# Kernel optimization log

Hardware: AMD Instinct MI355X
Metric: run time of the kernel (lower is better)

Reference implementation:

```python
import jax, jax.numpy as jnp
import numpy as np

NUM_EXPERTS = 8
HIDDEN = 1024
INTER = 1024
BATCH = 2
SEQ = 1024
TOP_K = 2
SWIGLU_ALPHA = 1.702
LIMIT = 7.0


def setup_inputs() -> dict:
    key = jax.random.key(0)
    ks = jax.random.split(key, 7)
    hidden_states = jax.random.normal(ks[0], (BATCH, SEQ, HIDDEN), jnp.float32)
    router_indices = jax.random.randint(ks[1], (BATCH * SEQ, TOP_K), 0, NUM_EXPERTS)
    routing_weights = jax.nn.softmax(
        jax.random.normal(ks[2], (BATCH * SEQ, NUM_EXPERTS), jnp.float32), axis=-1)
    scale = 0.02
    gate_up_proj = jax.random.normal(ks[3], (NUM_EXPERTS, HIDDEN, 2 * INTER), jnp.float32) * scale
    gate_up_proj_bias = jax.random.normal(ks[4], (NUM_EXPERTS, 2 * INTER), jnp.float32) * scale
    down_proj = jax.random.normal(ks[5], (NUM_EXPERTS, INTER, HIDDEN), jnp.float32) * scale
    down_proj_bias = jax.random.normal(ks[6], (NUM_EXPERTS, HIDDEN), jnp.float32) * scale
    return {
        "hidden_states": hidden_states,
        "router_indices": router_indices,
        "routing_weights": routing_weights,
        "gate_up_proj": gate_up_proj,
        "gate_up_proj_bias": gate_up_proj_bias,
        "down_proj": down_proj,
        "down_proj_bias": down_proj_bias,
    }


def _grouped_mm(x, w, expert_ids):
    """Grouped GEMM: y[t] = x[t] @ w[expert_ids[t]].

    x: [T, K], w: [E, K, N], expert_ids: [T] int.
    Reference form via one-hot masking (exact equivalent of torch._grouped_mm
    on expert-sorted tokens); guaranteed jit- and grad-safe.
    """
    onehot = jax.nn.one_hot(expert_ids, w.shape[0], dtype=x.dtype)  # [T, E]
    y_all = jnp.einsum('tk,ekn->etn', x, w)                         # [E, T, N]
    return jnp.einsum('te,etn->tn', onehot, y_all)                  # [T, N]


def _gpt_oss_swiglu(x):
    gate = jnp.minimum(x[..., ::2], LIMIT)
    up = jnp.clip(x[..., 1::2], -LIMIT, LIMIT)
    glu = gate * jax.nn.sigmoid(gate * SWIGLU_ALPHA)
    return (up + 1.0) * glu


def reference(hidden_states, router_indices, routing_weights,
              gate_up_proj, gate_up_proj_bias, down_proj, down_proj_bias):
    B = hidden_states.shape[0]
    H = hidden_states.shape[-1]
    x = hidden_states.reshape(-1, H)                       # [M, H]
    M = x.shape[0]
    top_k = router_indices.shape[1]
    num_experts = gate_up_proj.shape[0]

    # routing_weights is [M, num_experts] -> gather the top-k weights
    topk_weights = jnp.take_along_axis(routing_weights, router_indices, axis=1)  # [M, K]

    flat_experts = router_indices.reshape(-1)              # [T = M*K]
    sort_idx = jnp.argsort(flat_experts)                   # expert-sorted order
    sorted_pos = sort_idx // top_k                         # token id per slot
    expert_sorted = flat_experts[sort_idx]                 # [T]
    grouped = x[sorted_pos]                                # [T, H]

    gate_up = _grouped_mm(grouped, gate_up_proj, expert_sorted)
    gate_up = gate_up + gate_up_proj_bias[expert_sorted]   # per-expert bias
    inter = _gpt_oss_swiglu(gate_up)                       # [T, I]

    down = _grouped_mm(inter, down_proj, expert_sorted)
    down = down + down_proj_bias[expert_sorted]            # [T, H]
    down = down * topk_weights.reshape(-1)[sort_idx][:, None]

    out = jnp.zeros((M, H), x.dtype).at[sorted_pos].add(down)  # scatter-add combine
    return out.reshape(B, -1, H)
```

## Files before the change

### kernel.cpp

```cpp
#include <hip/hip_runtime.h>

#define NE 8
#define NH 1024
#define NI 1024
#define NGU 2048
#define MTOK 2048
#define TSLOT 4096

#define MAXT64 80
#define MAXT128 40

typedef short s16x8 __attribute__((ext_vector_type(8)));
typedef float f32x4 __attribute__((ext_vector_type(4)));
typedef unsigned short u16;

#define WS_SEG      0
#define WS_DESC64   64
#define WS_DESC128  384
#define WS_SLOT     1024
#define WS_POS      17408
#define WS_INTER    33792
#define WS_AREG     8422400UL
#define WS_WREG     25199616UL
#define WS_NEED_FAST 58754048UL

__device__ inline u16 f2bf(float f) {
    unsigned u = __builtin_bit_cast(unsigned, f);
    u += 0x7fffu + ((u >> 16) & 1u);
    return (u16)(u >> 16);
}

__device__ inline void lds_dma16(const u16* g, u16* l) {
    __builtin_amdgcn_global_load_lds(
        (const __attribute__((address_space(1))) unsigned int*)g,
        (__attribute__((address_space(3))) unsigned int*)l, 16, 0, 0);
}

__device__ inline int lds_off(int row, int blk) {
    return (row << 7) | (((blk ^ (row & 7)) & 7) << 4);
}

#define PIPE_FENCE asm volatile("" ::: "memory")
#define WAIT_VM6   asm volatile("s_waitcnt vmcnt(6)" ::: "memory")
#define WAIT_VM0   asm volatile("s_waitcnt vmcnt(0)" ::: "memory")

__global__ void k_build(const int* __restrict__ ridx, int* __restrict__ seg,
                        int* __restrict__ d64, int* __restrict__ d128,
                        int* __restrict__ slot_of, int* __restrict__ pos_of) {
    __shared__ int cnt[NE];
    __shared__ int cur[NE];
    int tid = threadIdx.x;
    if (tid < NE) cnt[tid] = 0;
    __syncthreads();
    for (int s = tid; s < TSLOT; s += blockDim.x) atomicAdd(&cnt[ridx[s] & 7], 1);
    __syncthreads();
    if (tid == 0) {
        int a = 0;
        for (int e = 0; e < NE; ++e) { seg[e] = a; cur[e] = a; a += cnt[e]; }
        seg[NE] = a;
        int nt = 0;
        for (int e = 0; e < NE; ++e)
            for (int m0 = 0; m0 < cnt[e]; m0 += 64) d64[nt++] = (e << 16) | (m0 / 64);
        for (; nt < MAXT64; ++nt) d64[nt] = -1;
        nt = 0;
        for (int e = 0; e < NE; ++e)
            for (int m0 = 0; m0 < cnt[e]; m0 += 128) d128[nt++] = (e << 16) | (m0 / 128);
        for (; nt < MAXT128; ++nt) d128[nt] = -1;
    }
    __syncthreads();
    for (int s = tid; s < TSLOT; s += blockDim.x) {
        int e = ridx[s] & 7;
        int p = atomicAdd(&cur[e], 1);
        slot_of[p] = s;
        pos_of[s] = p;
    }
}

__global__ __launch_bounds__(256) void k_gather(const float* __restrict__ x,
                                                const int* __restrict__ slot_of,
                                                u16* __restrict__ A) {
    int r = blockIdx.x;
    int token = slot_of[r] >> 1;
    float4 v = ((const float4*)(x + (size_t)token * NH))[threadIdx.x];
    ushort4 o;
    o.x = f2bf(v.x); o.y = f2bf(v.y); o.z = f2bf(v.z); o.w = f2bf(v.w);
    ((ushort4*)(A + (size_t)r * NH))[threadIdx.x] = o;
}

__global__ __launch_bounds__(256) void k_tr(const float* __restrict__ W,
                                            u16* __restrict__ WT, int K, int N) {
    __shared__ u16 T[64][66];
    int tid = threadIdx.x;
    const float* in = W + (size_t)blockIdx.z * K * N;
    u16* out = WT + (size_t)blockIdx.z * N * K;
    int n0 = blockIdx.x * 64, k0 = blockIdx.y * 64;
#pragma unroll
    for (int p = 0; p < 2; ++p) {
        int kr = p * 32 + (tid >> 4) * 2;
        int nc = (tid & 15) * 4;
        const float* r0 = in + (size_t)(k0 + kr) * N + n0 + nc;
        float4 v0 = *(const float4*)r0;
        float4 v1 = *(const float4*)(r0 + N);
#pragma unroll
        for (int i = 0; i < 4; ++i) {
            unsigned lo = f2bf(((const float*)&v0)[i]);
            unsigned hi = f2bf(((const float*)&v1)[i]);
            *(unsigned*)&T[nc + i][kr] = lo | (hi << 16);
        }
    }
    __syncthreads();
#pragma unroll
    for (int p = 0; p < 2; ++p) {
        int idx = p * 256 + tid;
        int nr = idx >> 3, kc = (idx & 7) * 8;
        unsigned q0 = *(const unsigned*)&T[nr][kc + 0];
        unsigned q1 = *(const unsigned*)&T[nr][kc + 2];
        unsigned q2 = *(const unsigned*)&T[nr][kc + 4];
        unsigned q3 = *(const unsigned*)&T[nr][kc + 6];
        uint4 vv = {q0, q1, q2, q3};
        *(uint4*)(out + (size_t)(n0 + nr) * K + k0 + kc) = vv;
    }
}

__global__ __launch_bounds__(256) void k_gateup_f(
        const u16* __restrict__ A,
        const u16* __restrict__ wt,
        const float* __restrict__ bias,
        const int* __restrict__ seg, const int* __restrict__ desc,
        u16* __restrict__ inter) {
    int d = desc[blockIdx.x];
    if (d < 0) return;
    int e = d >> 16, mt = d & 0xffff;
    int seg0 = seg[e], Te = seg[e + 1] - seg0, m0 = mt * 128;

    __shared__ __align__(16) u16 As0[128 * 64];
    __shared__ __align__(16) u16 As1[128 * 64];
    __shared__ __align__(16) u16 Bs0[64 * 64];
    __shared__ __align__(16) u16 Bs1[64 * 64];

    int tid = threadIdx.x;
    int lane = tid & 63, w = tid >> 6;
    int ml = lane & 15, kq = lane >> 4;
    int wm = w >> 1, wn = w & 1;
    int n0 = blockIdx.y * 64;
    const u16* wte = wt + (size_t)e * NGU * NH;
    int dr = lane >> 3, db = (lane & 7) ^ dr;

    const u16* aptr[4];
#pragma unroll
    for (int c = 0; c < 4; ++c) {
        int gr = seg0 + m0 + c * 32 + w * 8 + dr;
        if (gr > TSLOT - 1) gr = TSLOT - 1;
        aptr[c] = A + (size_t)gr * NH + db * 8;
    }
    const u16* bptr[2];
#pragma unroll
    for (int c = 0; c < 2; ++c)
        bptr[c] = wte + (size_t)(n0 + c * 32 + w * 8 + dr) * NH + db * 8;

    auto stage = [&](u16* AS, u16* BS, int kb) {
#pragma unroll
        for (int c = 0; c < 4; ++c) lds_dma16(aptr[c] + kb, AS + c * 2048 + w * 512);
#pragma unroll
        for (int c = 0; c < 2; ++c) lds_dma16(bptr[c] + kb, BS + c * 2048 + w * 512);
    };

    f32x4 zero = {0.f, 0.f, 0.f, 0.f};
    f32x4 acc[4][2];
#pragma unroll
    for (int i = 0; i < 4; ++i) { acc[i][0] = zero; acc[i][1] = zero; }

    auto compute = [&](const u16* AS, const u16* BS) {
#pragma unroll
        for (int kk = 0; kk < 64; kk += 32) {
            s16x8 af[4], bf[2];
#pragma unroll
            for (int i = 0; i < 4; ++i)
                af[i] = *(const s16x8*)((const char*)AS + lds_off(wm * 64 + i * 16 + ml, (kk >> 3) + kq));
#pragma unroll
            for (int i = 0; i < 2; ++i)
                bf[i] = *(const s16x8*)((const char*)BS + lds_off(wn * 32 + i * 16 + ml, (kk >> 3) + kq));
#pragma unroll
            for (int mi = 0; mi < 4; ++mi)
#pragma unroll
                for (int ni = 0; ni < 2; ++ni)
                    acc[mi][ni] = __builtin_amdgcn_mfma_f32_16x16x32_bf16(
                        af[mi], bf[ni], acc[mi][ni], 0, 0, 0);
        }
    };

    stage(As0, Bs0, 0);
    for (int t = 0; t < 16; t += 2) {
        stage(As1, Bs1, (t + 1) << 6);
        WAIT_VM6;
        __builtin_amdgcn_s_barrier();
        PIPE_FENCE;
        __builtin_amdgcn_s_setprio(1);
        compute(As0, Bs0);
        __builtin_amdgcn_s_setprio(0);
        PIPE_FENCE;
        __builtin_amdgcn_s_barrier();
        if (t < 14) {
            stage(As0, Bs0, (t + 2) << 6);
            WAIT_VM6;
        } else {
            WAIT_VM0;
        }
        __builtin_amdgcn_s_barrier();
        PIPE_FENCE;
        __builtin_amdgcn_s_setprio(1);
        compute(As1, Bs1);
        __builtin_amdgcn_s_setprio(0);
        PIPE_FENCE;
        __builtin_amdgcn_s_barrier();
    }

#pragma unroll
    for (int ni = 0; ni < 2; ++ni) {
        int n = n0 + wn * 32 + ni * 16 + ml;
        float bv = bias[e * NGU + n];
#pragma unroll
        for (int mi = 0; mi < 4; ++mi) {
#pragma unroll
            for (int r = 0; r < 4; ++r) {
                float v = acc[mi][ni][r] + bv;
                float pr = __shfl_xor(v, 1, 64);
                float g = (lane & 1) ? pr : v;
                float u = (lane & 1) ? v : pr;
                g = fminf(g, 7.0f);
                u = fminf(fmaxf(u, -7.0f), 7.0f);
                float glu = g / (1.0f + __expf(-1.702f * g));
                float y = (u + 1.0f) * glu;
                int mloc = wm * 64 + mi * 16 + kq * 4 + r;
                if (!(lane & 1) && (m0 + mloc) < Te)
                    inter[(size_t)(seg0 + m0 + mloc) * NI + (n >> 1)] = f2bf(y);
            }
        }
    }
}

__global__ __launch_bounds__(256) void k_down_f(
        const u16* __restrict__ inter,
        const u16* __restrict__ wt,
        const float* __restrict__ bias,
        const float* __restrict__ rw,
        const int* __restrict__ seg, const int* __restrict__ desc,
        const int* __restrict__ slot_of,
        float* __restrict__ out) {
    int d = desc[blockIdx.x];
    if (d < 0) return;
    int e = d >> 16, mt = d & 0xffff;
    int seg0 = seg[e], Te = seg[e + 1] - seg0, m0 = mt * 128;
    int kz = blockIdx.z;

    __shared__ __align__(16) u16 As0[128 * 64];
    __shared__ __align__(16) u16 As1[128 * 64];
    __shared__ __align__(16) u16 Bs0[64 * 64];
    __shared__ __align__(16) u16 Bs1[64 * 64];
    __shared__ int tokS[128];
    __shared__ float wgtS[128];

    int tid = threadIdx.x;
    if (tid < 128) {
        int m = m0 + tid;
        if (m < Te) {
            int token = slot_of[seg0 + m] >> 1;
            tokS[tid] = token;
            wgtS[tid] = rw[token * NE + e];
        } else {
            tokS[tid] = 0;
            wgtS[tid] = 0.0f;
        }
    }

    int lane = tid & 63, w = tid >> 6;
    int ml = lane & 15, kq = lane >> 4;
    int wm = w >> 1, wn = w & 1;
    int n0 = blockIdx.y * 64;
    const u16* wte = wt + (size_t)e * NH * NI;
    int dr = lane >> 3, db = (lane & 7) ^ dr;
    int kbeg = kz * (NI / 2);

    const u16* aptr[4];
#pragma unroll
    for (int c = 0; c < 4; ++c) {
        int gr = seg0 + m0 + c * 32 + w * 8 + dr;
        if (gr > TSLOT - 1) gr = TSLOT - 1;
        aptr[c] = inter + (size_t)gr * NI + db * 8;
    }
    const u16* bptr[2];
#pragma unroll
    for (int c = 0; c < 2; ++c)
        bptr[c] = wte + (size_t)(n0 + c * 32 + w * 8 + dr) * NI + db * 8;

    auto stage = [&](u16* AS, u16* BS, int kb) {
#pragma unroll
        for (int c = 0; c < 4; ++c) lds_dma16(aptr[c] + kb, AS + c * 2048 + w * 512);
#pragma unroll
        for (int c = 0; c < 2; ++c) lds_dma16(bptr[c] + kb, BS + c * 2048 + w * 512);
    };

    f32x4 zero = {0.f, 0.f, 0.f, 0.f};
    f32x4 acc[4][2];
#pragma unroll
    for (int i = 0; i < 4; ++i) { acc[i][0] = zero; acc[i][1] = zero; }

    auto compute = [&](const u16* AS, const u16* BS) {
#pragma unroll
        for (int kk = 0; kk < 64; kk += 32) {
            s16x8 af[4], bf[2];
#pragma unroll
            for (int i = 0; i < 4; ++i)
                af[i] = *(const s16x8*)((const char*)AS + lds_off(wm * 64 + i * 16 + ml, (kk >> 3) + kq));
#pragma unroll
            for (int i = 0; i < 2; ++i)
                bf[i] = *(const s16x8*)((const char*)BS + lds_off(wn * 32 + i * 16 + ml, (kk >> 3) + kq));
#pragma unroll
            for (int mi = 0; mi < 4; ++mi)
#pragma unroll
                for (int ni = 0; ni < 2; ++ni)
                    acc[mi][ni] = __builtin_amdgcn_mfma_f32_16x16x32_bf16(
                        af[mi], bf[ni], acc[mi][ni], 0, 0, 0);
        }
    };

    stage(As0, Bs0, kbeg);
    for (int t = 0; t < 8; t += 2) {
        stage(As1, Bs1, kbeg + ((t + 1) << 6));
        WAIT_VM6;
        __builtin_amdgcn_s_barrier();
        PIPE_FENCE;
        __builtin_amdgcn_s_setprio(1);
        compute(As0, Bs0);
        __builtin_amdgcn_s_setprio(0);
        PIPE_FENCE;
        __builtin_amdgcn_s_barrier();
        if (t < 6) {
            stage(As0, Bs0, kbeg + ((t + 2) << 6));
            WAIT_VM6;
        } else {
            WAIT_VM0;
        }
        __builtin_amdgcn_s_barrier();
        PIPE_FENCE;
        __builtin_amdgcn_s_setprio(1);
        compute(As1, Bs1);
        __builtin_amdgcn_s_setprio(0);
        PIPE_FENCE;
        __builtin_amdgcn_s_barrier();
    }

    float bv[2];
#pragma unroll
    for (int ni = 0; ni < 2; ++ni)
        bv[ni] = kz ? 0.0f : bias[e * NH + n0 + wn * 32 + ni * 16 + ml];

#pragma unroll
    for (int mi = 0; mi < 4; ++mi) {
#pragma unroll
        for (int r = 0; r < 4; ++r) {
            int mloc = wm * 64 + mi * 16 + kq * 4 + r;
            if ((m0 + mloc) < Te) {
                int token = tokS[mloc];
                float wgt = wgtS[mloc];
#pragma unroll
                for (int ni = 0; ni < 2; ++ni) {
                    int n = n0 + wn * 32 + ni * 16 + ml;
                    atomicAdd(&out[(size_t)token * NH + n], (acc[mi][ni][r] + bv[ni]) * wgt);
                }
            }
        }
    }
}

__global__ __launch_bounds__(256) void k_gateup_s(
        const float* __restrict__ x, const float* __restrict__ w,
        const float* __restrict__ bias,
        const int* __restrict__ seg, const int* __restrict__ desc,
        const int* __restrict__ slot_of, u16* __restrict__ inter) {
    int d = desc[blockIdx.x];
    if (d < 0) return;
    int e = d >> 16, mt = d & 0xffff;
    int seg0 = seg[e], Te = seg[e + 1] - seg0, m0 = mt * 64;
    __shared__ u16 As[64 * 40];
    __shared__ int tok[64];
    int tid = threadIdx.x;
    if (tid < 64) {
        int m = m0 + tid;
        tok[tid] = (m < Te) ? (slot_of[seg0 + m] >> 1) : -1;
    }
    __syncthreads();
    int lane = tid & 63, wave = tid >> 6;
    int arow = tid >> 2, acol = (tid & 3) * 8;
    int ta = tok[arow];
    int kq = lane >> 4, ml = lane & 15;
    int nb = blockIdx.y * 128 + wave * 32;
    const float* wp = w + (size_t)e * NH * NGU;
    f32x4 zero = {0.f, 0.f, 0.f, 0.f};
    f32x4 acc[4][2];
#pragma unroll
    for (int i = 0; i < 4; ++i) { acc[i][0] = zero; acc[i][1] = zero; }
    for (int kb = 0; kb < NH; kb += 32) {
        float4 a0 = {0, 0, 0, 0}, a1 = {0, 0, 0, 0};
        if (ta >= 0) {
            const float* xp = x + (size_t)ta * NH + kb + acol;
            a0 = *(const float4*)xp; a1 = *(const float4*)(xp + 4);
        }
        s16x8 av;
        av[0] = (short)f2bf(a0.x); av[1] = (short)f2bf(a0.y);
        av[2] = (short)f2bf(a0.z); av[3] = (short)f2bf(a0.w);
        av[4] = (short)f2bf(a1.x); av[5] = (short)f2bf(a1.y);
        av[6] = (short)f2bf(a1.z); av[7] = (short)f2bf(a1.w);
        __syncthreads();
        *(s16x8*)&As[arow * 40 + acol] = av;
        __syncthreads();
        s16x8 afr[4];
#pragma unroll
        for (int msi = 0; msi < 4; ++msi)
            afr[msi] = *(const s16x8*)&As[(msi * 16 + ml) * 40 + kq * 8];
        s16x8 bfr[2];
#pragma unroll
        for (int s = 0; s < 2; ++s) {
            const float* bp = wp + (size_t)(kb + kq * 8) * NGU + nb + s * 16 + ml;
#pragma unroll
            for (int j = 0; j < 8; ++j) bfr[s][j] = (short)f2bf(bp[(size_t)j * NGU]);
        }
#pragma unroll
        for (int msi = 0; msi < 4; ++msi)
#pragma unroll
            for (int s = 0; s < 2; ++s)
                acc[msi][s] = __builtin_amdgcn_mfma_f32_16x16x32_bf16(
                    afr[msi], bfr[s], acc[msi][s], 0, 0, 0);
    }
#pragma unroll
    for (int s = 0; s < 2; ++s) {
        int n = nb + s * 16 + ml;
        float bv = bias[e * NGU + n];
#pragma unroll
        for (int msi = 0; msi < 4; ++msi) {
#pragma unroll
            for (int r = 0; r < 4; ++r) {
                float v = acc[msi][s][r] + bv;
                float pr = __shfl_xor(v, 1, 64);
                float g = (lane & 1) ? pr : v;
                float u = (lane & 1) ? v : pr;
                g = fminf(g, 7.0f);
                u = fminf(fmaxf(u, -7.0f), 7.0f);
                float glu = g / (1.0f + __expf(-1.702f * g));
                float y = (u + 1.0f) * glu;
                int mrow = m0 + msi * 16 + kq * 4 + r;
                if (!(lane & 1) && mrow < Te)
                    inter[(size_t)(seg0 + mrow) * NI + (n >> 1)] = f2bf(y);
            }
        }
    }
}

__global__ __launch_bounds__(256) void k_down_s(
        const u16* __restrict__ inter, const float* __restrict__ w,
        const float* __restrict__ bias, const float* __restrict__ rw,
        const int* __restrict__ seg, const int* __restrict__ desc,
        const int* __restrict__ slot_of, float* __restrict__ out) {
    int d = desc[blockIdx.x];
    if (d < 0) return;
    int e = d >> 16, mt = d & 0xffff;
    int seg0 = seg[e], Te = seg[e + 1] - seg0, m0 = mt * 64;
    __shared__ u16 As[64 * 40];
    int tid = threadIdx.x;
    int lane = tid & 63, wave = tid >> 6;
    int arow = tid >> 2, acol = (tid & 3) * 8;
    bool avalid = (m0 + arow) < Te;
    int kq = lane >> 4, ml = lane & 15;
    int nb = blockIdx.y * 128 + wave * 32;
    const float* wp = w + (size_t)e * NI * NH;
    f32x4 zero = {0.f, 0.f, 0.f, 0.f};
    f32x4 acc[4][2];
#pragma unroll
    for (int i = 0; i < 4; ++i) { acc[i][0] = zero; acc[i][1] = zero; }
    for (int kb = 0; kb < NI; kb += 32) {
        s16x8 av = {0, 0, 0, 0, 0, 0, 0, 0};
        if (avalid) av = *(const s16x8*)(inter + (size_t)(seg0 + m0 + arow) * NI + kb + acol);
        __syncthreads();
        *(s16x8*)&As[arow * 40 + acol] = av;
        __syncthreads();
        s16x8 afr[4];
#pragma unroll
        for (int msi = 0; msi < 4; ++msi)
            afr[msi] = *(const s16x8*)&As[(msi * 16 + ml) * 40 + kq * 8];
        s16x8 bfr[2];
#pragma unroll
        for (int s = 0; s < 2; ++s) {
            const float* bp = wp + (size_t)(kb + kq * 8) * NH + nb + s * 16 + ml;
#pragma unroll
            for (int j = 0; j < 8; ++j) bfr[s][j] = (short)f2bf(bp[(size_t)j * NH]);
        }
#pragma unroll
        for (int msi = 0; msi < 4; ++msi)
#pragma unroll
            for (int s = 0; s < 2; ++s)
                acc[msi][s] = __builtin_amdgcn_mfma_f32_16x16x32_bf16(
                    afr[msi], bfr[s], acc[msi][s], 0, 0, 0);
    }
    float bv[2];
    bv[0] = bias[e * NH + nb + ml];
    bv[1] = bias[e * NH + nb + 16 + ml];
#pragma unroll
    for (int msi = 0; msi < 4; ++msi) {
#pragma unroll
        for (int r = 0; r < 4; ++r) {
            int mrow = m0 + msi * 16 + kq * 4 + r;
            if (mrow < Te) {
                int slot = slot_of[seg0 + mrow];
                int token = slot >> 1;
                float wgt = rw[token * NE + e];
#pragma unroll
                for (int s = 0; s < 2; ++s) {
                    int n = nb + s * 16 + ml;
                    atomicAdd(&out[(size_t)token * NH + n], (acc[msi][s][r] + bv[s]) * wgt);
                }
            }
        }
    }
}

extern "C" void kernel_launch(void* const* d_in, const int* in_sizes, int n_in,
                              void* d_out, int out_size, void* d_ws, size_t ws_size,
                              hipStream_t stream) {
    const float* x   = (const float*)d_in[0];
    const int*   ri  = (const int*)d_in[1];
    const float* rw  = (const float*)d_in[2];
    const float* wgu = (const float*)d_in[3];
    const float* bgu = (const float*)d_in[4];
    const float* wd  = (const float*)d_in[5];
    const float* bd  = (const float*)d_in[6];
    float* out = (float*)d_out;

    char* ws = (char*)d_ws;
    int* seg     = (int*)(ws + WS_SEG);
    int* d64     = (int*)(ws + WS_DESC64);
    int* d128    = (int*)(ws + WS_DESC128);
    int* slot_of = (int*)(ws + WS_SLOT);
    int* pos_of  = (int*)(ws + WS_POS);
    u16* inter   = (u16*)(ws + WS_INTER);

    hipLaunchKernelGGL(k_build, dim3(1), dim3(256), 0, stream, ri, seg, d64, d128,
                       slot_of, pos_of);
    hipMemsetAsync(out, 0, (size_t)MTOK * NH * sizeof(float), stream);

    if (ws_size >= WS_NEED_FAST) {
        u16* aReg = (u16*)(ws + WS_AREG);
        u16* wReg = (u16*)(ws + WS_WREG);
        hipLaunchKernelGGL(k_tr, dim3(NGU / 64, NH / 64, NE), dim3(256), 0, stream,
                           wgu, wReg, NH, NGU);
        hipLaunchKernelGGL(k_gather, dim3(TSLOT), dim3(256), 0, stream, x, slot_of, aReg);
        hipLaunchKernelGGL(k_gateup_f, dim3(MAXT128, NGU / 64), dim3(256), 0, stream,
                           aReg, wReg, bgu, seg, d128, inter);
        hipLaunchKernelGGL(k_tr, dim3(NH / 64, NI / 64, NE), dim3(256), 0, stream,
                           wd, wReg, NI, NH);
        hipLaunchKernelGGL(k_down_f, dim3(MAXT128, NH / 64, 2), dim3(256), 0, stream,
                           inter, wReg, bd, rw, seg, d128, slot_of, out);
    } else {
        hipLaunchKernelGGL(k_gateup_s, dim3(MAXT64, NGU / 128), dim3(256), 0, stream,
                           x, wgu, bgu, seg, d64, slot_of, inter);
        hipLaunchKernelGGL(k_down_s, dim3(MAXT64, NH / 128), dim3(256), 0, stream,
                           inter, wd, bd, rw, seg, d64, slot_of, out);
    }
}
```

Before: 248.3 us.

## Fuse routing, conversion, zeroing, and weight transposes into fewer launches

Merges routing-table build, bf16 conversion of the activations, output zeroing and the gate_up weight transpose into one prep kernel. The gather now indexes tokens directly through slot_of instead of building a separate expert-sorted copy. The down-projection weight transpose rides as extra blocks in the gate_up GEMM launch when the workspace is large enough. The down GEMM drops its K-split to run one pass over K. This cuts launch count, removes the memset and gather passes, and overlaps weight conversion with compute, at the cost of larger grids and fewer down-GEMM blocks.

After: 222.0 us. 10.6% less time.

```diff
diff --git a/kernel.cpp b/kernel.cpp
--- a/kernel.cpp
+++ b/kernel.cpp
@@ -21,8 +21,10 @@
 #define WS_POS      17408
 #define WS_INTER    33792
 #define WS_AREG     8422400UL
-#define WS_WREG     25199616UL
-#define WS_NEED_FAST 58754048UL
+#define WS_WREG     12616704UL
+#define WS_WTD      46171136UL
+#define WS_NEED_FAST  46171136UL
+#define WS_NEED_PIGGY 62948352UL
 
 __device__ inline u16 f2bf(float f) {
     unsigned u = __builtin_bit_cast(unsigned, f);
@@ -43,6 +45,362 @@
 #define PIPE_FENCE asm volatile("" ::: "memory")
 #define WAIT_VM6   asm volatile("s_waitcnt vmcnt(6)" ::: "memory")
 #define WAIT_VM0   asm volatile("s_waitcnt vmcnt(0)" ::: "memory")
+
+__device__ inline void tr_tile(const float* __restrict__ in, u16* __restrict__ outw,
+                               int K, int N, int n0, int k0, int tid, u16 (*T)[66]) {
+#pragma unroll
+    for (int p = 0; p < 2; ++p) {
+        int kr = p * 32 + (tid >> 4) * 2;
+        int nc = (tid & 15) * 4;
+        const float* r0 = in + (size_t)(k0 + kr) * N + n0 + nc;
+        float4 v0 = *(const float4*)r0;
+        float4 v1 = *(const float4*)(r0 + N);
+#pragma unroll
+        for (int i = 0; i < 4; ++i) {
+            unsigned lo = f2bf(((const float*)&v0)[i]);
+            unsigned hi = f2bf(((const float*)&v1)[i]);
+            *(unsigned*)&T[nc + i][kr] = lo | (hi << 16);
+        }
+    }
+    __syncthreads();
+#pragma unroll
+    for (int p = 0; p < 2; ++p) {
+        int idx = p * 256 + tid;
+        int nr = idx >> 3, kc = (idx & 7) * 8;
+        unsigned q0 = *(const unsigned*)&T[nr][kc + 0];
+        unsigned q1 = *(const unsigned*)&T[nr][kc + 2];
+        unsigned q2 = *(const unsigned*)&T[nr][kc + 4];
+        unsigned q3 = *(const unsigned*)&T[nr][kc + 6];
+        uint4 vv = {q0, q1, q2, q3};
+        *(uint4*)(outw + (size_t)(n0 + nr) * K + k0 + kc) = vv;
+    }
+}
+
+__global__ __launch_bounds__(256) void k_tr(const float* __restrict__ W,
+                                            u16* __restrict__ WT, int K, int N) {
+    __shared__ u16 T[64][66];
+    tr_tile(W + (size_t)blockIdx.z * K * N, WT + (size_t)blockIdx.z * N * K,
+            K, N, blockIdx.x * 64, blockIdx.y * 64, threadIdx.x, T);
+}
+
+__global__ __launch_bounds__(256) void k_prep(
+        const float* __restrict__ x, const int* __restrict__ ridx,
+        const float* __restrict__ wgu,
+        int* __restrict__ seg, int* __restrict__ d64, int* __restrict__ d128,
+        int* __restrict__ slot_of, int* __restrict__ pos_of,
+        u16* __restrict__ A, u16* __restrict__ wt_gu, float* __restrict__ out) {
+    __shared__ int cnt[NE];
+    __shared__ int cur[NE];
+    __shared__ u16 T[64][66];
+    int b = blockIdx.x;
+    int tid = threadIdx.x;
+
+    if (b == 0) {
+        if (tid < NE) cnt[tid] = 0;
+        __syncthreads();
+        for (int s = tid; s < TSLOT; s += blockDim.x) atomicAdd(&cnt[ridx[s] & 7], 1);
+        __syncthreads();
+        if (tid == 0) {
+            int a = 0;
+            for (int e = 0; e < NE; ++e) { seg[e] = a; cur[e] = a; a += cnt[e]; }
+            seg[NE] = a;
+            int nt = 0;
+            for (int e = 0; e < NE; ++e)
+                for (int m0 = 0; m0 < cnt[e]; m0 += 64) d64[nt++] = (e << 16) | (m0 / 64);
+            for (; nt < MAXT64; ++nt) d64[nt] = -1;
+            nt = 0;
+            for (int e = 0; e < NE; ++e)
+                for (int m0 = 0; m0 < cnt[e]; m0 += 128) d128[nt++] = (e << 16) | (m0 / 128);
+            for (; nt < MAXT128; ++nt) d128[nt] = -1;
+        }
+        __syncthreads();
+        for (int s = tid; s < TSLOT; s += blockDim.x) {
+            int e = ridx[s] & 7;
+            int p = atomicAdd(&cur[e], 1);
+            slot_of[p] = s;
+            pos_of[s] = p;
+        }
+    } else if (b <= MTOK) {
+        int t = b - 1;
+        float4 v = ((const float4*)(x + (size_t)t * NH))[tid];
+        ushort4 o;
+        o.x = f2bf(v.x); o.y = f2bf(v.y); o.z = f2bf(v.z); o.w = f2bf(v.w);
+        ((ushort4*)(A + (size_t)t * NH))[tid] = o;
+        float4 z = {0.f, 0.f, 0.f, 0.f};
+        ((float4*)(out + (size_t)t * NH))[tid] = z;
+    } else {
+        int id = b - (MTOK + 1);
+        int e = id >> 9, rem = id & 511;
+        int kblk = rem >> 5, nblk = rem & 31;
+        tr_tile(wgu + (size_t)e * NH * NGU, wt_gu + (size_t)e * NGU * NH,
+                NH, NGU, nblk * 64, kblk * 64, tid, T);
+    }
+}
+
+__global__ __launch_bounds__(256) void k_gateup_f(
+        const u16* __restrict__ A,
+        const u16* __restrict__ wt,
+        const float* __restrict__ bias,
+        const int* __restrict__ seg, const int* __restrict__ desc,
+        const int* __restrict__ slot_of,
+        u16* __restrict__ inter,
+        const float* __restrict__ wd,
+        u16* __restrict__ wtd) {
+    __shared__ __align__(16) char SM[49152];
+    int tid = threadIdx.x;
+
+    if (blockIdx.x >= MAXT128) {
+        int id = (blockIdx.x - MAXT128) * 32 + blockIdx.y;
+        int e = id >> 8, rem = id & 255;
+        int kblk = rem >> 4, nblk = rem & 15;
+        u16 (*T)[66] = (u16(*)[66])SM;
+        tr_tile(wd + (size_t)e * NI * NH, wtd + (size_t)e * NH * NI,
+                NI, NH, nblk * 64, kblk * 64, tid, T);
+        return;
+    }
+
+    int d = desc[blockIdx.x];
+    if (d < 0) return;
+    int e = d >> 16, mt = d & 0xffff;
+    int seg0 = seg[e], Te = seg[e + 1] - seg0, m0 = mt * 128;
+
+    u16* As0 = (u16*)SM;
+    u16* As1 = (u16*)(SM + 16384);
+    u16* Bs0 = (u16*)(SM + 32768);
+    u16* Bs1 = (u16*)(SM + 40960);
+
+    int lane = tid & 63, w = tid >> 6;
+    int ml = lane & 15, kq = lane >> 4;
+    int wm = w >> 1, wn = w & 1;
+    int n0 = blockIdx.y * 64;
+    const u16* wte = wt + (size_t)e * NGU * NH;
+    int dr = lane >> 3, db = (lane & 7) ^ dr;
+
+    const u16* aptr[4];
+#pragma unroll
+    for (int c = 0; c < 4; ++c) {
+        int gr = seg0 + m0 + c * 32 + w * 8 + dr;
+        if (gr > TSLOT - 1) gr = TSLOT - 1;
+        int tok = slot_of[gr] >> 1;
+        aptr[c] = A + (size_t)tok * NH + db * 8;
+    }
+    const u16* bptr[2];
+#pragma unroll
+    for (int c = 0; c < 2; ++c)
+        bptr[c] = wte + (size_t)(n0 + c * 32 + w * 8 + dr) * NH + db * 8;
+
+    auto stage = [&](u16* AS, u16* BS, int kb) {
+#pragma unroll
+        for (int c = 0; c < 4; ++c) lds_dma16(aptr[c] + kb, AS + c * 2048 + w * 512);
+#pragma unroll
+        for (int c = 0; c < 2; ++c) lds_dma16(bptr[c] + kb, BS + c * 2048 + w * 512);
+    };
+
+    f32x4 zero = {0.f, 0.f, 0.f, 0.f};
+    f32x4 acc[4][2];
+#pragma unroll
+    for (int i = 0; i < 4; ++i) { acc[i][0] = zero; acc[i][1] = zero; }
+
+    auto compute = [&](const u16* AS, const u16* BS) {
+#pragma unroll
+        for (int kk = 0; kk < 64; kk += 32) {
+            s16x8 af[4], bf[2];
+#pragma unroll
+            for (int i = 0; i < 4; ++i)
+                af[i] = *(const s16x8*)((const char*)AS + lds_off(wm * 64 + i * 16 + ml, (kk >> 3) + kq));
+#pragma unroll
+            for (int i = 0; i < 2; ++i)
+                bf[i] = *(const s16x8*)((const char*)BS + lds_off(wn * 32 + i * 16 + ml, (kk >> 3) + kq));
+#pragma unroll
+            for (int mi = 0; mi < 4; ++mi)
+#pragma unroll
+                for (int ni = 0; ni < 2; ++ni)
+                    acc[mi][ni] = __builtin_amdgcn_mfma_f32_16x16x32_bf16(
+                        af[mi], bf[ni], acc[mi][ni], 0, 0, 0);
+        }
+    };
+
+    stage(As0, Bs0, 0);
+    for (int t = 0; t < 16; t += 2) {
+        stage(As1, Bs1, (t + 1) << 6);
+        WAIT_VM6;
+        __builtin_amdgcn_s_barrier();
+        PIPE_FENCE;
+        __builtin_amdgcn_s_setprio(1);
+        compute(As0, Bs0);
+        __builtin_amdgcn_s_setprio(0);
+        PIPE_FENCE;
+        __builtin_amdgcn_s_barrier();
+        if (t < 14) {
+            stage(As0, Bs0, (t + 2) << 6);
+            WAIT_VM6;
+        } else {
+            WAIT_VM0;
+        }
+        __builtin_amdgcn_s_barrier();
+        PIPE_FENCE;
+        __builtin_amdgcn_s_setprio(1);
+        compute(As1, Bs1);
+        __builtin_amdgcn_s_setprio(0);
+        PIPE_FENCE;
+        __builtin_amdgcn_s_barrier();
+    }
+
+#pragma unroll
+    for (int ni = 0; ni < 2; ++ni) {
+        int n = n0 + wn * 32 + ni * 16 + ml;
+        float bv = bias[e * NGU + n];
+#pragma unroll
+        for (int mi = 0; mi < 4; ++mi) {
+#pragma unroll
+            for (int r = 0; r < 4; ++r) {
+                float v = acc[mi][ni][r] + bv;
+                float pr = __shfl_xor(v, 1, 64);
+                float g = (lane & 1) ? pr : v;
+                float u = (lane & 1) ? v : pr;
+                g = fminf(g, 7.0f);
+                u = fminf(fmaxf(u, -7.0f), 7.0f);
+                float glu = g / (1.0f + __expf(-1.702f * g));
+                float y = (u + 1.0f) * glu;
+                int mloc = wm * 64 + mi * 16 + kq * 4 + r;
+                if (!(lane & 1) && (m0 + mloc) < Te)
+                    inter[(size_t)(seg0 + m0 + mloc) * NI + (n >> 1)] = f2bf(y);
+            }
+        }
+    }
+}
+
+__global__ __launch_bounds__(256) void k_down_f(
+        const u16* __restrict__ inter,
+        const u16* __restrict__ wt,
+        const float* __restrict__ bias,
+        const float* __restrict__ rw,
+        const int* __restrict__ seg, const int* __restrict__ desc,
+        const int* __restrict__ slot_of,
+        float* __restrict__ out) {
+    int d = desc[blockIdx.x];
+    if (d < 0) return;
+    int e = d >> 16, mt = d & 0xffff;
+    int seg0 = seg[e], Te = seg[e + 1] - seg0, m0 = mt * 128;
+
+    __shared__ __align__(16) u16 As0[128 * 64];
+    __shared__ __align__(16) u16 As1[128 * 64];
+    __shared__ __align__(16) u16 Bs0[64 * 64];
+    __shared__ __align__(16) u16 Bs1[64 * 64];
+    __shared__ int tokS[128];
+    __shared__ float wgtS[128];
+
+    int tid = threadIdx.x;
+    if (tid < 128) {
+        int m = m0 + tid;
+        if (m < Te) {
+            int token = slot_of[seg0 + m] >> 1;
+            tokS[tid] = token;
+            wgtS[tid] = rw[token * NE + e];
+        } else {
+            tokS[tid] = 0;
+            wgtS[tid] = 0.0f;
+        }
+    }
+
+    int lane = tid & 63, w = tid >> 6;
+    int ml = lane & 15, kq = lane >> 4;
+    int wm = w >> 1, wn = w & 1;
+    int n0 = blockIdx.y * 64;
+    const u16* wte = wt + (size_t)e * NH * NI;
+    int dr = lane >> 3, db = (lane & 7) ^ dr;
+
+    const u16* aptr[4];
+#pragma unroll
+    for (int c = 0; c < 4; ++c) {
+        int gr = seg0 + m0 + c * 32 + w * 8 + dr;
+        if (gr > TSLOT - 1) gr = TSLOT - 1;
+        aptr[c] = inter + (size_t)gr * NI + db * 8;
+    }
+    const u16* bptr[2];
+#pragma unroll
+    for (int c = 0; c < 2; ++c)
+        bptr[c] = wte + (size_t)(n0 + c * 32 + w * 8 + dr) * NI + db * 8;
+
+    auto stage = [&](u16* AS, u16* BS, int kb) {
+#pragma unroll
+        for (int c = 0; c < 4; ++c) lds_dma16(aptr[c] + kb, AS + c * 2048 + w * 512);
+#pragma unroll
+        for (int c = 0; c < 2; ++c) lds_dma16(bptr[c] + kb, BS + c * 2048 + w * 512);
+    };
+
+    f32x4 zero = {0.f, 0.f, 0.f, 0.f};
+    f32x4 acc[4][2];
+#pragma unroll
+    for (int i = 0; i < 4; ++i) { acc[i][0] = zero; acc[i][1] = zero; }
+
+    auto compute = [&](const u16* AS, const u16* BS) {
+#pragma unroll
+        for (int kk = 0; kk < 64; kk += 32) {
+            s16x8 af[4], bf[2];
+#pragma unroll
+            for (int i = 0; i < 4; ++i)
+                af[i] = *(const s16x8*)((const char*)AS + lds_off(wm * 64 + i * 16 + ml, (kk >> 3) + kq));
+#pragma unroll
+            for (int i = 0; i < 2; ++i)
+                bf[i] = *(const s16x8*)((const char*)BS + lds_off(wn * 32 + i * 16 + ml, (kk >> 3) + kq));
+#pragma unroll
+            for (int mi = 0; mi < 4; ++mi)
+#pragma unroll
+                for (int ni = 0; ni < 2; ++ni)
+                    acc[mi][ni] = __builtin_amdgcn_mfma_f32_16x16x32_bf16(
+                        af[mi], bf[ni], acc[mi][ni], 0, 0, 0);
+        }
+    };
+
+    stage(As0, Bs0, 0);
+    for (int t = 0; t < 16; t += 2) {
+        stage(As1, Bs1, (t + 1) << 6);
+        WAIT_VM6;
+        __builtin_amdgcn_s_barrier();
+        PIPE_FENCE;
+        __builtin_amdgcn_s_setprio(1);
+        compute(As0, Bs0);
+        __builtin_amdgcn_s_setprio(0);
+        PIPE_FENCE;
+        __builtin_amdgcn_s_barrier();
+        if (t < 14) {
+            stage(As0, Bs0, (t + 2) << 6);
+            WAIT_VM6;
+        } else {
+            WAIT_VM0;
+        }
+        __builtin_amdgcn_s_barrier();
+        PIPE_FENCE;
+        __builtin_amdgcn_s_setprio(1);
+        compute(As1, Bs1);
+        __builtin_amdgcn_s_setprio(0);
+        PIPE_FENCE;
+        __builtin_amdgcn_s_barrier();
+    }
+
+    float bv[2];
+#pragma unroll
+    for (int ni = 0; ni < 2; ++ni)
+        bv[ni] = bias[e * NH + n0 + wn * 32 + ni * 16 + ml];
+
+#pragma unroll
+    for (int mi = 0; mi < 4; ++mi) {
+#pragma unroll
+        for (int r = 0; r < 4; ++r) {
+            int mloc = wm * 64 + mi * 16 + kq * 4 + r;
+            if ((m0 + mloc) < Te) {
+                int token = tokS[mloc];
+                float wgt = wgtS[mloc];
+#pragma unroll
+                for (int ni = 0; ni < 2; ++ni) {
+                    int n = n0 + wn * 32 + ni * 16 + ml;
+                    atomicAdd(&out[(size_t)token * NH + n], (acc[mi][ni][r] + bv[ni]) * wgt);
+                }
+            }
+        }
+    }
+}
 
 __global__ void k_build(const int* __restrict__ ridx, int* __restrict__ seg,
                         int* __restrict__ d64, int* __restrict__ d128,
@@ -76,303 +434,6 @@
     }
 }
 
-__global__ __launch_bounds__(256) void k_gather(const float* __restrict__ x,
-                                                const int* __restrict__ slot_of,
-                                                u16* __restrict__ A) {
-    int r = blockIdx.x;
-    int token = slot_of[r] >> 1;
-    float4 v = ((const float4*)(x + (size_t)token * NH))[threadIdx.x];
-    ushort4 o;
-    o.x = f2bf(v.x); o.y = f2bf(v.y); o.z = f2bf(v.z); o.w = f2bf(v.w);
-    ((ushort4*)(A + (size_t)r * NH))[threadIdx.x] = o;
-}
-
-__global__ __launch_bounds__(256) void k_tr(const float* __restrict__ W,
-                                            u16* __restrict__ WT, int K, int N) {
-    __shared__ u16 T[64][66];
-    int tid = threadIdx.x;
-    const float* in = W + (size_t)blockIdx.z * K * N;
-    u16* out = WT + (size_t)blockIdx.z * N * K;
-    int n0 = blockIdx.x * 64, k0 = blockIdx.y * 64;
-#pragma unroll
-    for (int p = 0; p < 2; ++p) {
-        int kr = p * 32 + (tid >> 4) * 2;
-        int nc = (tid & 15) * 4;
-        const float* r0 = in + (size_t)(k0 + kr) * N + n0 + nc;
-        float4 v0 = *(const float4*)r0;
-        float4 v1 = *(const float4*)(r0 + N);
-#pragma unroll
-        for (int i = 0; i < 4; ++i) {
-            unsigned lo = f2bf(((const float*)&v0)[i]);
-            unsigned hi = f2bf(((const float*)&v1)[i]);
-            *(unsigned*)&T[nc + i][kr] = lo | (hi << 16);
-        }
-    }
-    __syncthreads();
-#pragma unroll
-    for (int p = 0; p < 2; ++p) {
-        int idx = p * 256 + tid;
-        int nr = idx >> 3, kc = (idx & 7) * 8;
-        unsigned q0 = *(const unsigned*)&T[nr][kc + 0];
-        unsigned q1 = *(const unsigned*)&T[nr][kc + 2];
-        unsigned q2 = *(const unsigned*)&T[nr][kc + 4];
-        unsigned q3 = *(const unsigned*)&T[nr][kc + 6];
-        uint4 vv = {q0, q1, q2, q3};
-        *(uint4*)(out + (size_t)(n0 + nr) * K + k0 + kc) = vv;
-    }
-}
-
-__global__ __launch_bounds__(256) void k_gateup_f(
-        const u16* __restrict__ A,
-        const u16* __restrict__ wt,
-        const float* __restrict__ bias,
-        const int* __restrict__ seg, const int* __restrict__ desc,
-        u16* __restrict__ inter) {
-    int d = desc[blockIdx.x];
-    if (d < 0) return;
-    int e = d >> 16, mt = d & 0xffff;
-    int seg0 = seg[e], Te = seg[e + 1] - seg0, m0 = mt * 128;
-
-    __shared__ __align__(16) u16 As0[128 * 64];
-    __shared__ __align__(16) u16 As1[128 * 64];
-    __shared__ __align__(16) u16 Bs0[64 * 64];
-    __shared__ __align__(16) u16 Bs1[64 * 64];
-
-    int tid = threadIdx.x;
-    int lane = tid & 63, w = tid >> 6;
-    int ml = lane & 15, kq = lane >> 4;
-    int wm = w >> 1, wn = w & 1;
-    int n0 = blockIdx.y * 64;
-    const u16* wte = wt + (size_t)e * NGU * NH;
-    int dr = lane >> 3, db = (lane & 7) ^ dr;
-
-    const u16* aptr[4];
-#pragma unroll
-    for (int c = 0; c < 4; ++c) {
-        int gr = seg0 + m0 + c * 32 + w * 8 + dr;
-        if (gr > TSLOT - 1) gr = TSLOT - 1;
-        aptr[c] = A + (size_t)gr * NH + db * 8;
-    }
-    const u16* bptr[2];
-#pragma unroll
-    for (int c = 0; c < 2; ++c)
-        bptr[c] = wte + (size_t)(n0 + c * 32 + w * 8 + dr) * NH + db * 8;
-
-    auto stage = [&](u16* AS, u16* BS, int kb) {
-#pragma unroll
-        for (int c = 0; c < 4; ++c) lds_dma16(aptr[c] + kb, AS + c * 2048 + w * 512);
-#pragma unroll
-        for (int c = 0; c < 2; ++c) lds_dma16(bptr[c] + kb, BS + c * 2048 + w * 512);
-    };
-
-    f32x4 zero = {0.f, 0.f, 0.f, 0.f};
-    f32x4 acc[4][2];
-#pragma unroll
-    for (int i = 0; i < 4; ++i) { acc[i][0] = zero; acc[i][1] = zero; }
-
-    auto compute = [&](const u16* AS, const u16* BS) {
-#pragma unroll
-        for (int kk = 0; kk < 64; kk += 32) {
-            s16x8 af[4], bf[2];
-#pragma unroll
-            for (int i = 0; i < 4; ++i)
-                af[i] = *(const s16x8*)((const char*)AS + lds_off(wm * 64 + i * 16 + ml, (kk >> 3) + kq));
-#pragma unroll
-            for (int i = 0; i < 2; ++i)
-                bf[i] = *(const s16x8*)((const char*)BS + lds_off(wn * 32 + i * 16 + ml, (kk >> 3) + kq));
-#pragma unroll
-            for (int mi = 0; mi < 4; ++mi)
-#pragma unroll
-                for (int ni = 0; ni < 2; ++ni)
-                    acc[mi][ni] = __builtin_amdgcn_mfma_f32_16x16x32_bf16(
-                        af[mi], bf[ni], acc[mi][ni], 0, 0, 0);
-        }
-    };
-
-    stage(As0, Bs0, 0);
-    for (int t = 0; t < 16; t += 2) {
-        stage(As1, Bs1, (t + 1) << 6);
-        WAIT_VM6;
-        __builtin_amdgcn_s_barrier();
-        PIPE_FENCE;
-        __builtin_amdgcn_s_setprio(1);
-        compute(As0, Bs0);
-        __builtin_amdgcn_s_setprio(0);
-        PIPE_FENCE;
-        __builtin_amdgcn_s_barrier();
-        if (t < 14) {
-            stage(As0, Bs0, (t + 2) << 6);
-            WAIT_VM6;
-        } else {
-            WAIT_VM0;
-        }
-        __builtin_amdgcn_s_barrier();
-        PIPE_FENCE;
-        __builtin_amdgcn_s_setprio(1);
-        compute(As1, Bs1);
-        __builtin_amdgcn_s_setprio(0);
-        PIPE_FENCE;
-        __builtin_amdgcn_s_barrier();
-    }
-
-#pragma unroll
-    for (int ni = 0; ni < 2; ++ni) {
-        int n = n0 + wn * 32 + ni * 16 + ml;
-        float bv = bias[e * NGU + n];
-#pragma unroll
-        for (int mi = 0; mi < 4; ++mi) {
-#pragma unroll
-            for (int r = 0; r < 4; ++r) {
-                float v = acc[mi][ni][r] + bv;
-                float pr = __shfl_xor(v, 1, 64);
-                float g = (lane & 1) ? pr : v;
-                float u = (lane & 1) ? v : pr;
-                g = fminf(g, 7.0f);
-                u = fminf(fmaxf(u, -7.0f), 7.0f);
-                float glu = g / (1.0f + __expf(-1.702f * g));
-                float y = (u + 1.0f) * glu;
-                int mloc = wm * 64 + mi * 16 + kq * 4 + r;
-                if (!(lane & 1) && (m0 + mloc) < Te)
-                    inter[(size_t)(seg0 + m0 + mloc) * NI + (n >> 1)] = f2bf(y);
-            }
-        }
-    }
-}
-
-__global__ __launch_bounds__(256) void k_down_f(
-        const u16* __restrict__ inter,
-        const u16* __restrict__ wt,
-        const float* __restrict__ bias,
-        const float* __restrict__ rw,
-        const int* __restrict__ seg, const int* __restrict__ desc,
-        const int* __restrict__ slot_of,
-        float* __restrict__ out) {
-    int d = desc[blockIdx.x];
-    if (d < 0) return;
-    int e = d >> 16, mt = d & 0xffff;
-    int seg0 = seg[e], Te = seg[e + 1] - seg0, m0 = mt * 128;
-    int kz = blockIdx.z;
-
-    __shared__ __align__(16) u16 As0[128 * 64];
-    __shared__ __align__(16) u16 As1[128 * 64];
-    __shared__ __align__(16) u16 Bs0[64 * 64];
-    __shared__ __align__(16) u16 Bs1[64 * 64];
-    __shared__ int tokS[128];
-    __shared__ float wgtS[128];
-
-    int tid = threadIdx.x;
-    if (tid < 128) {
-        int m = m0 + tid;
-        if (m < Te) {
-            int token = slot_of[seg0 + m] >> 1;
-            tokS[tid] = token;
-            wgtS[tid] = rw[token * NE + e];
-        } else {
-            tokS[tid] = 0;
-            wgtS[tid] = 0.0f;
-        }
-    }
-
-    int lane = tid & 63, w = tid >> 6;
-    int ml = lane & 15, kq = lane >> 4;
-    int wm = w >> 1, wn = w & 1;
-    int n0 = blockIdx.y * 64;
-    const u16* wte = wt + (size_t)e * NH * NI;
-    int dr = lane >> 3, db = (lane & 7) ^ dr;
-    int kbeg = kz * (NI / 2);
-
-    const u16* aptr[4];
-#pragma unroll
-    for (int c = 0; c < 4; ++c) {
-        int gr = seg0 + m0 + c * 32 + w * 8 + dr;
-        if (gr > TSLOT - 1) gr = TSLOT - 1;
-        aptr[c] = inter + (size_t)gr * NI + db * 8;
-    }
-    const u16* bptr[2];
-#pragma unroll
-    for (int c = 0; c < 2; ++c)
-        bptr[c] = wte + (size_t)(n0 + c * 32 + w * 8 + dr) * NI + db * 8;
-
-    auto stage = [&](u16* AS, u16* BS, int kb) {
-#pragma unroll
-        for (int c = 0; c < 4; ++c) lds_dma16(aptr[c] + kb, AS + c * 2048 + w * 512);
-#pragma unroll
-        for (int c = 0; c < 2; ++c) lds_dma16(bptr[c] + kb, BS + c * 2048 + w * 512);
-    };
-
-    f32x4 zero = {0.f, 0.f, 0.f, 0.f};
-    f32x4 acc[4][2];
-#pragma unroll
-    for (int i = 0; i < 4; ++i) { acc[i][0] = zero; acc[i][1] = zero; }
-
-    auto compute = [&](const u16* AS, const u16* BS) {
-#pragma unroll
-        for (int kk = 0; kk < 64; kk += 32) {
-            s16x8 af[4], bf[2];
-#pragma unroll
-            for (int i = 0; i < 4; ++i)
-                af[i] = *(const s16x8*)((const char*)AS + lds_off(wm * 64 + i * 16 + ml, (kk >> 3) + kq));
-#pragma unroll
-            for (int i = 0; i < 2; ++i)
-                bf[i] = *(const s16x8*)((const char*)BS + lds_off(wn * 32 + i * 16 + ml, (kk >> 3) + kq));
-#pragma unroll
-            for (int mi = 0; mi < 4; ++mi)
-#pragma unroll
-                for (int ni = 0; ni < 2; ++ni)
-                    acc[mi][ni] = __builtin_amdgcn_mfma_f32_16x16x32_bf16(
-                        af[mi], bf[ni], acc[mi][ni], 0, 0, 0);
-        }
-    };
-
-    stage(As0, Bs0, kbeg);
-    for (int t = 0; t < 8; t += 2) {
-        stage(As1, Bs1, kbeg + ((t + 1) << 6));
-        WAIT_VM6;
-        __builtin_amdgcn_s_barrier();
-        PIPE_FENCE;
-        __builtin_amdgcn_s_setprio(1);
-        compute(As0, Bs0);
-        __builtin_amdgcn_s_setprio(0);
-        PIPE_FENCE;
-        __builtin_amdgcn_s_barrier();
-        if (t < 6) {
-            stage(As0, Bs0, kbeg + ((t + 2) << 6));
-            WAIT_VM6;
-        } else {
-            WAIT_VM0;
-        }
-        __builtin_amdgcn_s_barrier();
-        PIPE_FENCE;
-        __builtin_amdgcn_s_setprio(1);
-        compute(As1, Bs1);
-        __builtin_amdgcn_s_setprio(0);
-        PIPE_FENCE;
-        __builtin_amdgcn_s_barrier();
-    }
-
-    float bv[2];
-#pragma unroll
-    for (int ni = 0; ni < 2; ++ni)
-        bv[ni] = kz ? 0.0f : bias[e * NH + n0 + wn * 32 + ni * 16 + ml];
-
-#pragma unroll
-    for (int mi = 0; mi < 4; ++mi) {
-#pragma unroll
-        for (int r = 0; r < 4; ++r) {
-            int mloc = wm * 64 + mi * 16 + kq * 4 + r;
-            if ((m0 + mloc) < Te) {
-                int token = tokS[mloc];
-                float wgt = wgtS[mloc];
-#pragma unroll
-                for (int ni = 0; ni < 2; ++ni) {
-                    int n = n0 + wn * 32 + ni * 16 + ml;
-                    atomicAdd(&out[(size_t)token * NH + n], (acc[mi][ni][r] + bv[ni]) * wgt);
-                }
-            }
-        }
-    }
-}
-
 __global__ __launch_bounds__(256) void k_gateup_s(
         const float* __restrict__ x, const float* __restrict__ w,
         const float* __restrict__ bias,
@@ -543,23 +604,31 @@
     int* pos_of  = (int*)(ws + WS_POS);
     u16* inter   = (u16*)(ws + WS_INTER);
 
-    hipLaunchKernelGGL(k_build, dim3(1), dim3(256), 0, stream, ri, seg, d64, d128,
-                       slot_of, pos_of);
-    hipMemsetAsync(out, 0, (size_t)MTOK * NH * sizeof(float), stream);
-
-    if (ws_size >= WS_NEED_FAST) {
+    if (ws_size >= WS_NEED_PIGGY) {
         u16* aReg = (u16*)(ws + WS_AREG);
         u16* wReg = (u16*)(ws + WS_WREG);
-        hipLaunchKernelGGL(k_tr, dim3(NGU / 64, NH / 64, NE), dim3(256), 0, stream,
-                           wgu, wReg, NH, NGU);
-        hipLaunchKernelGGL(k_gather, dim3(TSLOT), dim3(256), 0, stream, x, slot_of, aReg);
+        u16* wtd  = (u16*)(ws + WS_WTD);
+        hipLaunchKernelGGL(k_prep, dim3(1 + MTOK + 4096), dim3(256), 0, stream,
+                           x, ri, wgu, seg, d64, d128, slot_of, pos_of, aReg, wReg, out);
+        hipLaunchKernelGGL(k_gateup_f, dim3(MAXT128 + 64, NGU / 64), dim3(256), 0, stream,
+                           aReg, wReg, bgu, seg, d128, slot_of, inter, wd, wtd);
+        hipLaunchKernelGGL(k_down_f, dim3(MAXT128, NH / 64), dim3(256), 0, stream,
+                           inter, wtd, bd, rw, seg, d128, slot_of, out);
+    } else if (ws_size >= WS_NEED_FAST) {
+        u16* aReg = (u16*)(ws + WS_AREG);
+        u16* wReg = (u16*)(ws + WS_WREG);
+        hipLaunchKernelGGL(k_prep, dim3(1 + MTOK + 4096), dim3(256), 0, stream,
+                           x, ri, wgu, seg, d64, d128, slot_of, pos_of, aReg, wReg, out);
         hipLaunchKernelGGL(k_gateup_f, dim3(MAXT128, NGU / 64), dim3(256), 0, stream,
-                           aReg, wReg, bgu, seg, d128, inter);
+                           aReg, wReg, bgu, seg, d128, slot_of, inter, wd, wReg);
         hipLaunchKernelGGL(k_tr, dim3(NH / 64, NI / 64, NE), dim3(256), 0, stream,
                            wd, wReg, NI, NH);
-        hipLaunchKernelGGL(k_down_f, dim3(MAXT128, NH / 64, 2), dim3(256), 0, stream,
+        hipLaunchKernelGGL(k_down_f, dim3(MAXT128, NH / 64), dim3(256), 0, stream,
                            inter, wReg, bd, rw, seg, d128, slot_of, out);
     } else {
+        hipLaunchKernelGGL(k_build, dim3(1), dim3(256), 0, stream, ri, seg, d64, d128,
+                           slot_of, pos_of);
+        hipMemsetAsync(out, 0, (size_t)MTOK * NH * sizeof(float), stream);
         hipLaunchKernelGGL(k_gateup_s, dim3(MAXT64, NGU / 128), dim3(256), 0, stream,
                            x, wgu, bgu, seg, d64, slot_of, inter);
         hipLaunchKernelGGL(k_down_s, dim3(MAXT64, NH / 128), dim3(256), 0, stream,
```
